# Optimization experiments

Hardware: AMD Instinct MI355X
Metric: run time of the kernel (lower is better)

Reference implementation:

```python
import jax, jax.numpy as jnp
import numpy as np

B, LQ, LK, D, H = 4, 2048, 2048, 768, 12
DH = D // H  # 64
EPS = 1e-5


def setup_inputs() -> dict:
    key = jax.random.key(0)
    ks = jax.random.split(key, 12)
    s = 0.02
    return {
        "queries": jax.random.normal(ks[0], (B, LQ, D), jnp.float32),
        "keys": jax.random.normal(ks[1], (B, LK, D), jnp.float32),
        "values": jax.random.normal(ks[2], (B, LK, D), jnp.float32),
        "mask": jax.random.randint(ks[3], (B, LK), 0, 2, jnp.int32),
        "Wq": jax.random.normal(ks[4], (D, D), jnp.float32) * s,
        "Wk": jax.random.normal(ks[5], (D, D), jnp.float32) * s,
        "Wv": jax.random.normal(ks[6], (D, D), jnp.float32) * s,
        "Wo": jax.random.normal(ks[7], (D, D), jnp.float32) * s,
        "W1": jax.random.normal(ks[8], (D, D), jnp.float32) * s,
        "b1": jnp.zeros((D,), jnp.float32),
        "W2": jax.random.normal(ks[9], (D, D), jnp.float32) * s,
        "b2": jnp.zeros((D,), jnp.float32),
        "ln_g": jnp.ones((D,), jnp.float32),
        "ln_b": jnp.zeros((D,), jnp.float32),
    }


def _split_heads(x):
    # [B, L, D] -> [B, H, L, DH]
    b, l, _ = x.shape
    return x.reshape(b, l, H, DH).transpose(0, 2, 1, 3)


def reference(queries, keys, values, mask, Wq, Wk, Wv, Wo, W1, b1, W2, b2, ln_g, ln_b):
    q = _split_heads(queries @ Wq)  # [B,H,LQ,DH]
    k = _split_heads(keys @ Wk)     # [B,H,LK,DH]
    v = _split_heads(values @ Wv)   # [B,H,LK,DH]

    scores = jnp.einsum("bhqd,bhkd->bhqk", q, k) / jnp.sqrt(jnp.float32(DH))

    # valid length per batch row = count of nonzero mask entries; positions >= valid_len are masked
    valid_lens = jnp.sum(mask != 0, axis=1)  # [B]
    key_ok = jnp.arange(LK, dtype=jnp.int32)[None, :] < valid_lens[:, None]  # [B,LK]
    scores = jnp.where(key_ok[:, None, None, :], scores, jnp.float32(-1e6))

    attn = jax.nn.softmax(scores, axis=-1)  # dropout is identity in eval
    out = jnp.einsum("bhqk,bhkd->bhqd", attn, v)  # [B,H,LQ,DH]
    out = out.transpose(0, 2, 1, 3).reshape(out.shape[0], out.shape[2], D)

    att_out = out @ Wo  # [B,LQ,D]
    ffn = jax.nn.relu(att_out @ W1 + b1) @ W2 + b2

    # residual + layernorm (torch code intends ln(dropout(ffn) + att_out))
    y = ffn + att_out
    mu = jnp.mean(y, axis=-1, keepdims=True)
    var = jnp.mean(jnp.square(y - mu), axis=-1, keepdims=True)
    return (y - mu) / jnp.sqrt(var + EPS) * ln_g + ln_b
```

## Files before the change

### kernel.cpp

```cpp
#include <hip/hip_runtime.h>
#include <stdint.h>

typedef __attribute__((ext_vector_type(4))) float floatx4;
typedef __attribute__((ext_vector_type(8))) __bf16 bf16x8;
typedef __attribute__((ext_vector_type(4))) __bf16 bf16x4;

#define DEV __device__ __forceinline__

constexpr int HB = 12;
constexpr int LSEQ = 2048;
constexpr int DMODEL = 768;
constexpr int MROWS = 8192;
constexpr float QSCALE = 0.125f * 1.44269504088896f;

DEV short f2bf(float f) {
  union { float f; uint32_t u; } x; x.f = f;
  uint32_t r = x.u + 0x7FFFu + ((x.u >> 16) & 1u);
  return (short)(r >> 16);
}

DEV float bf2f(short s) {
  union { uint32_t u; float f; } x; x.u = ((uint32_t)(uint16_t)s) << 16;
  return x.f;
}

typedef __attribute__((address_space(1))) void as1_void;
typedef __attribute__((address_space(3))) void as3_void;

DEV void gload_lds16(const void* g, void* l) {
  __builtin_amdgcn_global_load_lds((as1_void*)(uintptr_t)g, (as3_void*)l, 16, 0, 0);
}

__global__ __launch_bounds__(256)
void transpose_k(const float* w0, const float* w1, const float* w2,
                 const float* w3, const float* w4, const float* w5,
                 short* o0, short* o1, short* o2, short* o3, short* o4, short* o5)
{
  const float* W; short* O;
  switch (blockIdx.z) {
    case 0: W = w0; O = o0; break;
    case 1: W = w1; O = o1; break;
    case 2: W = w2; O = o2; break;
    case 3: W = w3; O = o3; break;
    case 4: W = w4; O = o4; break;
    default: W = w5; O = o5; break;
  }
  __shared__ float t[32][33];
  const int tx = threadIdx.x & 31, ty = threadIdx.x >> 5;
  const int n0 = blockIdx.x * 32, k0 = blockIdx.y * 32;
#pragma unroll
  for (int i = 0; i < 4; ++i)
    t[ty + i * 8][tx] = W[(size_t)(k0 + ty + i * 8) * DMODEL + n0 + tx];
  __syncthreads();
#pragma unroll
  for (int i = 0; i < 4; ++i)
    O[(size_t)(n0 + ty + i * 8) * DMODEL + k0 + tx] = f2bf(t[tx][ty + i * 8]);
}

__global__ __launch_bounds__(256)
void cvt_k(const float* __restrict__ s0, const float* __restrict__ s1, const float* __restrict__ s2,
           short* __restrict__ d0, short* __restrict__ d1, short* __restrict__ d2)
{
  const float* s; short* d;
  switch (blockIdx.y) { case 0: s = s0; d = d0; break; case 1: s = s1; d = d1; break; default: s = s2; d = d2; break; }
  const size_t i = ((size_t)blockIdx.x * 256 + threadIdx.x) * 4;
  const float4 v = *(const float4*)(s + i);
  short4 r; r.x = f2bf(v.x); r.y = f2bf(v.y); r.z = f2bf(v.z); r.w = f2bf(v.w);
  *(short4*)(d + i) = r;
}

__global__ __launch_bounds__(256)
void vlens_k(const int* __restrict__ mask, int* __restrict__ vl)
{
  const int b = blockIdx.x;
  int s = 0;
  for (int i = threadIdx.x; i < LSEQ; i += 256) s += (mask[b * LSEQ + i] != 0) ? 1 : 0;
#pragma unroll
  for (int o = 32; o >= 1; o >>= 1) s += __shfl_xor(s, o);
  __shared__ int red[4];
  const int lane = threadIdx.x & 63, wave = threadIdx.x >> 6;
  if (lane == 0) red[wave] = s;
  __syncthreads();
  if (threadIdx.x == 0) vl[b] = red[0] + red[1] + red[2] + red[3];
}

enum { EPI_QKV = 0, EPI_PLAIN = 2, EPI_BIAS_RELU = 3, EPI_Y = 4 };

template <int EPI>
__global__ __launch_bounds__(256)
void gemm_k(const short* __restrict__ A0, const short* __restrict__ A1, const short* __restrict__ A2,
            const short* __restrict__ B0, const short* __restrict__ B1, const short* __restrict__ B2,
            const float* __restrict__ bias, const short* __restrict__ resid,
            void* __restrict__ o0, void* __restrict__ o1, void* __restrict__ o2)
{
  __shared__ __align__(16) short As[2][2][64 * 32];
  __shared__ __align__(16) short Bs[2][2][128 * 32];
  const short* A = A0;
  const short* Bt = B0;
  if constexpr (EPI == EPI_QKV) {
    if (blockIdx.z == 1) { A = A1; Bt = B1; }
    else if (blockIdx.z == 2) { A = A2; Bt = B2; }
  }
  const int tid = threadIdx.x;
  const int lane = tid & 63, wave = tid >> 6;
  const int wm = wave >> 1, wn = wave & 1;
  const int m0 = blockIdx.x * 64, n0 = blockIdx.y * 128;
  const int col = lane & 15, quad = lane >> 4;
  const int sr = lane >> 2;
  const int sk = (lane & 3) * 8;

  const short* Arow = A + (size_t)(m0 + wave * 16 + sr) * DMODEL + sk;
  const short* Brow0 = Bt + (size_t)(n0 + (wave * 2 + 0) * 16 + sr) * DMODEL + sk;
  const short* Brow1 = Bt + (size_t)(n0 + (wave * 2 + 1) * 16 + sr) * DMODEL + sk;

  auto stage = [&](int kt, int buf) {
    const int k0 = kt * 64;
#pragma unroll
    for (int h = 0; h < 2; ++h) {
      gload_lds16(Arow + k0 + h * 32, &As[buf][h][wave * 512]);
      gload_lds16(Brow0 + k0 + h * 32, &Bs[buf][h][(wave * 2 + 0) * 512]);
      gload_lds16(Brow1 + k0 + h * 32, &Bs[buf][h][(wave * 2 + 1) * 512]);
    }
  };

  floatx4 acc[2][4] = {};

  stage(0, 0);
  for (int kt = 0; kt < 12; ++kt) {
    const int cur = kt & 1;
    asm volatile("s_barrier" ::: "memory");
    if (kt + 1 < 12) {
      stage(kt + 1, cur ^ 1);
      asm volatile("s_waitcnt vmcnt(6)" ::: "memory");
    } else {
      asm volatile("s_waitcnt vmcnt(0)" ::: "memory");
    }
    asm volatile("s_barrier" ::: "memory");
#pragma unroll
    for (int h = 0; h < 2; ++h) {
      bf16x8 af[2], bfr[4];
#pragma unroll
      for (int t = 0; t < 2; ++t)
        af[t] = *(const bf16x8*)&As[cur][h][(wm * 32 + t * 16 + col) * 32 + quad * 8];
#pragma unroll
      for (int t = 0; t < 4; ++t)
        bfr[t] = *(const bf16x8*)&Bs[cur][h][(wn * 64 + t * 16 + col) * 32 + quad * 8];
#pragma unroll
      for (int mt = 0; mt < 2; ++mt)
#pragma unroll
        for (int nt = 0; nt < 4; ++nt)
          acc[mt][nt] = __builtin_amdgcn_mfma_f32_16x16x32_bf16(af[mt], bfr[nt], acc[mt][nt], 0, 0, 0);
    }
  }

#pragma unroll
  for (int mt = 0; mt < 2; ++mt) {
#pragma unroll
    for (int nt = 0; nt < 4; ++nt) {
#pragma unroll
      for (int r = 0; r < 4; ++r) {
        const int m = m0 + wm * 32 + mt * 16 + quad * 4 + r;
        const int n = n0 + wn * 64 + nt * 16 + col;
        float v = acc[mt][nt][r];
        if constexpr (EPI == EPI_QKV) {
          const int b = m >> 11, l = m & 2047, h = n >> 6, dh = n & 63;
          const int z = blockIdx.z;
          if (z == 0) {
            ((short*)o0)[((size_t)(b * HB + h) * LSEQ + l) * 64 + dh] = f2bf(v * QSCALE);
          } else if (z == 1) {
            ((short*)o1)[((size_t)(b * HB + h) * LSEQ + l) * 64 + dh] = f2bf(v);
          } else {
            ((short*)o2)[((size_t)(b * HB + h) * 64 + dh) * LSEQ + l] = f2bf(v);
          }
        } else if constexpr (EPI == EPI_PLAIN) {
          ((short*)o0)[(size_t)m * DMODEL + n] = f2bf(v);
        } else if constexpr (EPI == EPI_BIAS_RELU) {
          v += bias[n]; v = v > 0.f ? v : 0.f;
          ((short*)o0)[(size_t)m * DMODEL + n] = f2bf(v);
        } else {
          v += bias[n] + bf2f(resid[(size_t)m * DMODEL + n]);
          ((float*)o0)[(size_t)m * DMODEL + n] = v;
        }
      }
    }
  }
}

constexpr int PSP = 68;
__global__ __launch_bounds__(256)
void attn_k(const short* __restrict__ qw, const short* __restrict__ kw, const short* __restrict__ vtw,
            const int* __restrict__ vlens, short* __restrict__ outp)
{
  __shared__ __align__(16) short Qs[2][128][32];
  __shared__ __align__(16) short Ks[2][64][32];
  __shared__ __align__(16) short Vts[2][64][32];
  __shared__ __align__(16) short Ps[4][32 * PSP];

  const int tid = threadIdx.x;
  const int lane = tid & 63, wave = tid >> 6;
  const int col = lane & 15, quad = lane >> 4;
  const int bh = blockIdx.x, b = bh / HB, h = bh % HB;
  const int q0 = blockIdx.y * 128;
  const int vl = vlens[b];
  const int sr = lane >> 2, sk = (lane & 3) * 8;

  const short* qbase = qw  + (size_t)bh * LSEQ * 64;
  const short* kbase = kw  + (size_t)bh * LSEQ * 64;
  const short* vbase = vtw + (size_t)bh * 64 * LSEQ;

#pragma unroll
  for (int i = 0; i < 4; ++i) {
    const int c = wave * 4 + i;
    const int hs = c >> 3, r0 = (c & 7) * 16;
    gload_lds16(qbase + (size_t)(q0 + r0 + sr) * 64 + hs * 32 + sk, &Qs[hs][r0][0]);
  }

  floatx4 oacc[2][4] = {};
  float li[2][4] = {};

  const int ktend = (vl > 0) ? ((vl + 63) >> 6) : (LSEQ / 64);

  for (int kt = 0; kt < ktend; ++kt) {
    __syncthreads();
#pragma unroll
    for (int i = 0; i < 2; ++i) {
      const int c = wave * 2 + i;
      const int hs = c >> 2, r0 = (c & 3) * 16;
      gload_lds16(kbase + (size_t)(kt * 64 + r0 + sr) * 64 + hs * 32 + sk, &Ks[hs][r0][0]);
      gload_lds16(vbase + (size_t)(r0 + sr) * LSEQ + kt * 64 + hs * 32 + sk, &Vts[hs][r0][0]);
    }
    __syncthreads();

    floatx4 sacc[2][4] = {};
#pragma unroll
    for (int ks = 0; ks < 2; ++ks) {
      bf16x8 aq[2], bk[4];
#pragma unroll
      for (int mt = 0; mt < 2; ++mt)
        aq[mt] = *(const bf16x8*)&Qs[ks][wave * 32 + mt * 16 + col][quad * 8];
#pragma unroll
      for (int nt = 0; nt < 4; ++nt)
        bk[nt] = *(const bf16x8*)&Ks[ks][nt * 16 + col][quad * 8];
#pragma unroll
      for (int mt = 0; mt < 2; ++mt)
#pragma unroll
        for (int nt = 0; nt < 4; ++nt)
          sacc[mt][nt] = __builtin_amdgcn_mfma_f32_16x16x32_bf16(aq[mt], bk[nt], sacc[mt][nt], 0, 0, 0);
    }

    if (kt * 64 + 64 > vl) {
#pragma unroll
      for (int nt = 0; nt < 4; ++nt) {
        const bool ok = (kt * 64 + nt * 16 + col) < vl;
#pragma unroll
        for (int mt = 0; mt < 2; ++mt)
#pragma unroll
          for (int r = 0; r < 4; ++r)
            sacc[mt][nt][r] = ok ? sacc[mt][nt][r] : -1.0e6f;
      }
    }

#pragma unroll
    for (int mt = 0; mt < 2; ++mt)
#pragma unroll
      for (int nt = 0; nt < 4; ++nt)
#pragma unroll
        for (int r = 0; r < 4; ++r) {
          const float p = __builtin_amdgcn_exp2f(sacc[mt][nt][r]);
          li[mt][r] += p;
          union { float f; uint32_t u; } pu; pu.f = p;
          Ps[wave][(mt * 16 + quad * 4 + r) * PSP + nt * 16 + col] =
              (short)((pu.u + 0x8000u) >> 16);
        }

    asm volatile("s_waitcnt lgkmcnt(0)" ::: "memory");

#pragma unroll
    for (int ks = 0; ks < 2; ++ks) {
      bf16x8 ap[2], bv[4];
#pragma unroll
      for (int mt = 0; mt < 2; ++mt) {
        union { bf16x8 v8; bf16x4 v4[2]; } u;
        const short* base = &Ps[wave][(mt * 16 + col) * PSP + ks * 32 + quad * 8];
        u.v4[0] = *(const bf16x4*)base;
        u.v4[1] = *(const bf16x4*)(base + 4);
        ap[mt] = u.v8;
      }
#pragma unroll
      for (int nt = 0; nt < 4; ++nt)
        bv[nt] = *(const bf16x8*)&Vts[ks][nt * 16 + col][quad * 8];
#pragma unroll
      for (int mt = 0; mt < 2; ++mt)
#pragma unroll
        for (int nt = 0; nt < 4; ++nt)
          oacc[mt][nt] = __builtin_amdgcn_mfma_f32_16x16x32_bf16(ap[mt], bv[nt], oacc[mt][nt], 0, 0, 0);
    }
  }

  float rli[2][4];
#pragma unroll
  for (int mt = 0; mt < 2; ++mt)
#pragma unroll
    for (int r = 0; r < 4; ++r) {
      float t = li[mt][r];
      t += __shfl_xor(t, 1); t += __shfl_xor(t, 2);
      t += __shfl_xor(t, 4); t += __shfl_xor(t, 8);
      rli[mt][r] = 1.0f / fmaxf(t, 1e-30f);
    }

#pragma unroll
  for (int mt = 0; mt < 2; ++mt)
#pragma unroll
    for (int nt = 0; nt < 4; ++nt)
#pragma unroll
      for (int r = 0; r < 4; ++r) {
        const int qrow = q0 + wave * 32 + mt * 16 + quad * 4 + r;
        const int dh = nt * 16 + col;
        const float v = oacc[mt][nt][r] * rli[mt][r];
        outp[((size_t)b * LSEQ + qrow) * DMODEL + h * 64 + dh] = f2bf(v);
      }
}

__global__ __launch_bounds__(256)
void ln_k(const float* __restrict__ y, const float* __restrict__ g, const float* __restrict__ be,
          float* __restrict__ o)
{
  const int row = blockIdx.x;
  const int tid = threadIdx.x;
  const float* yr = y + (size_t)row * DMODEL;
  float v[3];
  float s = 0.f, sq = 0.f;
#pragma unroll
  for (int i = 0; i < 3; ++i) { v[i] = yr[tid + i * 256]; s += v[i]; sq += v[i] * v[i]; }
#pragma unroll
  for (int off = 32; off >= 1; off >>= 1) { s += __shfl_xor(s, off); sq += __shfl_xor(sq, off); }
  __shared__ float red[8];
  const int lane = tid & 63, wave = tid >> 6;
  if (lane == 0) { red[wave] = s; red[4 + wave] = sq; }
  __syncthreads();
  s = red[0] + red[1] + red[2] + red[3];
  sq = red[4] + red[5] + red[6] + red[7];
  const float mu = s * (1.f / 768.f);
  const float var = sq * (1.f / 768.f) - mu * mu;
  const float rstd = rsqrtf(var + 1e-5f);
  float* orow = o + (size_t)row * DMODEL;
#pragma unroll
  for (int i = 0; i < 3; ++i) {
    const int c = tid + i * 256;
    orow[c] = (v[i] - mu) * rstd * g[c] + be[c];
  }
}

extern "C" void kernel_launch(void* const* d_in, const int* in_sizes, int n_in,
                              void* d_out, int out_size, void* d_ws, size_t ws_size,
                              hipStream_t stream)
{
  const float* queries = (const float*)d_in[0];
  const float* keys    = (const float*)d_in[1];
  const float* values  = (const float*)d_in[2];
  const int*   mask    = (const int*)d_in[3];
  const float* Wq = (const float*)d_in[4];
  const float* Wk = (const float*)d_in[5];
  const float* Wv = (const float*)d_in[6];
  const float* Wo = (const float*)d_in[7];
  const float* W1 = (const float*)d_in[8];
  const float* b1 = (const float*)d_in[9];
  const float* W2 = (const float*)d_in[10];
  const float* b2 = (const float*)d_in[11];
  const float* ln_g = (const float*)d_in[12];
  const float* ln_b = (const float*)d_in[13];

  char* ws = (char*)d_ws;
  size_t off = 0;
  auto alloc = [&](size_t bytes) -> void* {
    void* p = ws + off;
    off = (off + bytes + 255) & ~(size_t)255;
    return p;
  };
  int* vlens = (int*)alloc(256);
  short* wt[6];
  for (int i = 0; i < 6; ++i) wt[i] = (short*)alloc((size_t)DMODEL * DMODEL * 2);
  constexpr size_t SB = (size_t)MROWS * DMODEL * 2;
  short* xq  = (short*)alloc(SB);
  short* xk  = (short*)alloc(SB);
  short* xv  = (short*)alloc(SB);
  short* qw  = (short*)alloc(SB);
  short* kw  = (short*)alloc(SB);
  short* vtw = (short*)alloc(SB);
  short* attn_cat = xq;
  short* atto_bf  = xk;
  short* h1       = xv;
  float* yb       = (float*)qw;

  dim3 blk(256);
  transpose_k<<<dim3(24, 24, 6), blk, 0, stream>>>(Wq, Wk, Wv, Wo, W1, W2,
                                                   wt[0], wt[1], wt[2], wt[3], wt[4], wt[5]);
  cvt_k<<<dim3(6144, 3), blk, 0, stream>>>(queries, keys, values, xq, xk, xv);
  vlens_k<<<dim3(4), blk, 0, stream>>>(mask, vlens);
  gemm_k<EPI_QKV><<<dim3(128, 6, 3), blk, 0, stream>>>(
      xq, xk, xv, wt[0], wt[1], wt[2], nullptr, nullptr, qw, kw, vtw);
  attn_k<<<dim3(48, 16), blk, 0, stream>>>(qw, kw, vtw, vlens, attn_cat);
  gemm_k<EPI_PLAIN><<<dim3(128, 6, 1), blk, 0, stream>>>(
      attn_cat, nullptr, nullptr, wt[3], nullptr, nullptr, nullptr, nullptr,
      atto_bf, nullptr, nullptr);
  gemm_k<EPI_BIAS_RELU><<<dim3(128, 6, 1), blk, 0, stream>>>(
      atto_bf, nullptr, nullptr, wt[4], nullptr, nullptr, b1, nullptr,
      h1, nullptr, nullptr);
  gemm_k<EPI_Y><<<dim3(128, 6, 1), blk, 0, stream>>>(
      h1, nullptr, nullptr, wt[5], nullptr, nullptr, b2, atto_bf,
      yb, nullptr, nullptr);
  ln_k<<<dim3(MROWS), blk, 0, stream>>>(yb, ln_g, ln_b, (float*)d_out);
}
```

Baseline: 332.6 us.

## Keep P in registers via transposed S MFMA and double-buffer K/V tiles

The attention kernel now computes S transposed (K as the A operand, Q as B), so each lane holds four consecutive keys for one query. Those values are packed to bf16 and fed straight into 16x16x16 MFMAs against V^T, which removes the P round-trip through shared memory. K/V tiles are double-buffered with a prefetch of the next tile and raw barriers plus vmcnt waits, so global loads overlap with compute. Output is stored as 4-wide vectors. The risks are the smaller-K MFMA (more instructions), higher register pressure, and the correctness of the hand-placed waitcnt and barrier sequence.

```diff
diff --git a/kernel.cpp b/kernel.cpp
--- a/kernel.cpp
+++ b/kernel.cpp
@@ -3,7 +3,7 @@
 
 typedef __attribute__((ext_vector_type(4))) float floatx4;
 typedef __attribute__((ext_vector_type(8))) __bf16 bf16x8;
-typedef __attribute__((ext_vector_type(4))) __bf16 bf16x4;
+typedef __attribute__((ext_vector_type(4))) short short4v;
 
 #define DEV __device__ __forceinline__
 
@@ -186,15 +186,13 @@
   }
 }
 
-constexpr int PSP = 68;
 __global__ __launch_bounds__(256)
 void attn_k(const short* __restrict__ qw, const short* __restrict__ kw, const short* __restrict__ vtw,
             const int* __restrict__ vlens, short* __restrict__ outp)
 {
   __shared__ __align__(16) short Qs[2][128][32];
-  __shared__ __align__(16) short Ks[2][64][32];
-  __shared__ __align__(16) short Vts[2][64][32];
-  __shared__ __align__(16) short Ps[4][32 * PSP];
+  __shared__ __align__(16) short Ks[2][2][64][32];
+  __shared__ __align__(16) short Vts[2][2][64][32];
 
   const int tid = threadIdx.x;
   const int lane = tid & 63, wave = tid >> 6;
@@ -215,110 +213,118 @@
     gload_lds16(qbase + (size_t)(q0 + r0 + sr) * 64 + hs * 32 + sk, &Qs[hs][r0][0]);
   }
 
-  floatx4 oacc[2][4] = {};
-  float li[2][4] = {};
-
-  const int ktend = (vl > 0) ? ((vl + 63) >> 6) : (LSEQ / 64);
-
-  for (int kt = 0; kt < ktend; ++kt) {
-    __syncthreads();
+  auto stage = [&](int kt, int buf) {
 #pragma unroll
     for (int i = 0; i < 2; ++i) {
       const int c = wave * 2 + i;
       const int hs = c >> 2, r0 = (c & 3) * 16;
-      gload_lds16(kbase + (size_t)(kt * 64 + r0 + sr) * 64 + hs * 32 + sk, &Ks[hs][r0][0]);
-      gload_lds16(vbase + (size_t)(r0 + sr) * LSEQ + kt * 64 + hs * 32 + sk, &Vts[hs][r0][0]);
-    }
-    __syncthreads();
-
-    floatx4 sacc[2][4] = {};
+      gload_lds16(kbase + (size_t)(kt * 64 + r0 + sr) * 64 + hs * 32 + sk, &Ks[buf][hs][r0][0]);
+      gload_lds16(vbase + (size_t)(r0 + sr) * LSEQ + kt * 64 + hs * 32 + sk, &Vts[buf][hs][r0][0]);
+    }
+  };
+
+  floatx4 oacc[4][2] = {};
+  float li[2] = {};
+
+  const int ktend = (vl > 0) ? ((vl + 63) >> 6) : (LSEQ / 64);
+
+  stage(0, 0);
+  for (int kt = 0; kt < ktend; ++kt) {
+    const int cur = kt & 1;
+    asm volatile("s_barrier" ::: "memory");
+    if (kt + 1 < ktend) {
+      stage(kt + 1, cur ^ 1);
+      asm volatile("s_waitcnt vmcnt(4)" ::: "memory");
+    } else {
+      asm volatile("s_waitcnt vmcnt(0)" ::: "memory");
+    }
+    asm volatile("s_barrier" ::: "memory");
+
+    floatx4 sacc[4][2] = {};
 #pragma unroll
     for (int ks = 0; ks < 2; ++ks) {
-      bf16x8 aq[2], bk[4];
-#pragma unroll
-      for (int mt = 0; mt < 2; ++mt)
-        aq[mt] = *(const bf16x8*)&Qs[ks][wave * 32 + mt * 16 + col][quad * 8];
-#pragma unroll
-      for (int nt = 0; nt < 4; ++nt)
-        bk[nt] = *(const bf16x8*)&Ks[ks][nt * 16 + col][quad * 8];
-#pragma unroll
-      for (int mt = 0; mt < 2; ++mt)
-#pragma unroll
-        for (int nt = 0; nt < 4; ++nt)
-          sacc[mt][nt] = __builtin_amdgcn_mfma_f32_16x16x32_bf16(aq[mt], bk[nt], sacc[mt][nt], 0, 0, 0);
+      bf16x8 kf[4], qf[2];
+#pragma unroll
+      for (int kc = 0; kc < 4; ++kc)
+        kf[kc] = *(const bf16x8*)&Ks[cur][ks][kc * 16 + col][quad * 8];
+#pragma unroll
+      for (int qc = 0; qc < 2; ++qc)
+        qf[qc] = *(const bf16x8*)&Qs[ks][wave * 32 + qc * 16 + col][quad * 8];
+#pragma unroll
+      for (int kc = 0; kc < 4; ++kc)
+#pragma unroll
+        for (int qc = 0; qc < 2; ++qc)
+          sacc[kc][qc] = __builtin_amdgcn_mfma_f32_16x16x32_bf16(kf[kc], qf[qc], sacc[kc][qc], 0, 0, 0);
     }
 
     if (kt * 64 + 64 > vl) {
 #pragma unroll
-      for (int nt = 0; nt < 4; ++nt) {
-        const bool ok = (kt * 64 + nt * 16 + col) < vl;
-#pragma unroll
-        for (int mt = 0; mt < 2; ++mt)
-#pragma unroll
-          for (int r = 0; r < 4; ++r)
-            sacc[mt][nt][r] = ok ? sacc[mt][nt][r] : -1.0e6f;
+      for (int kc = 0; kc < 4; ++kc) {
+        const int pbase = kt * 64 + kc * 16 + quad * 4;
+#pragma unroll
+        for (int r = 0; r < 4; ++r) {
+          const bool ok = (pbase + r) < vl;
+#pragma unroll
+          for (int qc = 0; qc < 2; ++qc)
+            sacc[kc][qc][r] = ok ? sacc[kc][qc][r] : -1.0e6f;
+        }
       }
     }
 
-#pragma unroll
-    for (int mt = 0; mt < 2; ++mt)
-#pragma unroll
-      for (int nt = 0; nt < 4; ++nt)
-#pragma unroll
-        for (int r = 0; r < 4; ++r) {
-          const float p = __builtin_amdgcn_exp2f(sacc[mt][nt][r]);
-          li[mt][r] += p;
-          union { float f; uint32_t u; } pu; pu.f = p;
-          Ps[wave][(mt * 16 + quad * 4 + r) * PSP + nt * 16 + col] =
-              (short)((pu.u + 0x8000u) >> 16);
-        }
-
-    asm volatile("s_waitcnt lgkmcnt(0)" ::: "memory");
-
-#pragma unroll
-    for (int ks = 0; ks < 2; ++ks) {
-      bf16x8 ap[2], bv[4];
-#pragma unroll
-      for (int mt = 0; mt < 2; ++mt) {
-        union { bf16x8 v8; bf16x4 v4[2]; } u;
-        const short* base = &Ps[wave][(mt * 16 + col) * PSP + ks * 32 + quad * 8];
-        u.v4[0] = *(const bf16x4*)base;
-        u.v4[1] = *(const bf16x4*)(base + 4);
-        ap[mt] = u.v8;
+    short4v pf[4][2];
+#pragma unroll
+    for (int kc = 0; kc < 4; ++kc)
+#pragma unroll
+      for (int qc = 0; qc < 2; ++qc) {
+        union { float f; uint32_t u; } p0, p1, p2, p3;
+        p0.f = __builtin_amdgcn_exp2f(sacc[kc][qc][0]);
+        p1.f = __builtin_amdgcn_exp2f(sacc[kc][qc][1]);
+        p2.f = __builtin_amdgcn_exp2f(sacc[kc][qc][2]);
+        p3.f = __builtin_amdgcn_exp2f(sacc[kc][qc][3]);
+        li[qc] += (p0.f + p1.f) + (p2.f + p3.f);
+        union { int2 i2; short4v s4; } pk;
+        pk.i2.x = (int)__builtin_amdgcn_perm(p1.u, p0.u, 0x07060302u);
+        pk.i2.y = (int)__builtin_amdgcn_perm(p3.u, p2.u, 0x07060302u);
+        pf[kc][qc] = pk.s4;
       }
-#pragma unroll
-      for (int nt = 0; nt < 4; ++nt)
-        bv[nt] = *(const bf16x8*)&Vts[ks][nt * 16 + col][quad * 8];
-#pragma unroll
-      for (int mt = 0; mt < 2; ++mt)
-#pragma unroll
-        for (int nt = 0; nt < 4; ++nt)
-          oacc[mt][nt] = __builtin_amdgcn_mfma_f32_16x16x32_bf16(ap[mt], bv[nt], oacc[mt][nt], 0, 0, 0);
-    }
-  }
-
-  float rli[2][4];
-#pragma unroll
-  for (int mt = 0; mt < 2; ++mt)
-#pragma unroll
-    for (int r = 0; r < 4; ++r) {
-      float t = li[mt][r];
-      t += __shfl_xor(t, 1); t += __shfl_xor(t, 2);
-      t += __shfl_xor(t, 4); t += __shfl_xor(t, 8);
-      rli[mt][r] = 1.0f / fmaxf(t, 1e-30f);
-    }
-
-#pragma unroll
-  for (int mt = 0; mt < 2; ++mt)
-#pragma unroll
-    for (int nt = 0; nt < 4; ++nt)
-#pragma unroll
-      for (int r = 0; r < 4; ++r) {
-        const int qrow = q0 + wave * 32 + mt * 16 + quad * 4 + r;
-        const int dh = nt * 16 + col;
-        const float v = oacc[mt][nt][r] * rli[mt][r];
-        outp[((size_t)b * LSEQ + qrow) * DMODEL + h * 64 + dh] = f2bf(v);
-      }
+
+#pragma unroll
+    for (int nt = 0; nt < 4; ++nt) {
+      short4v vf[4];
+#pragma unroll
+      for (int kc = 0; kc < 4; ++kc)
+        vf[kc] = *(const short4v*)&Vts[cur][kc >> 1][nt * 16 + col][(kc & 1) * 16 + quad * 4];
+#pragma unroll
+      for (int qc = 0; qc < 2; ++qc)
+#pragma unroll
+        for (int kc = 0; kc < 4; ++kc)
+          oacc[nt][qc] = __builtin_amdgcn_mfma_f32_16x16x16bf16_1k(vf[kc], pf[kc][qc], oacc[nt][qc], 0, 0, 0);
+    }
+  }
+
+  float rli[2];
+#pragma unroll
+  for (int qc = 0; qc < 2; ++qc) {
+    float t = li[qc];
+    t += __shfl_xor(t, 16);
+    t += __shfl_xor(t, 32);
+    rli[qc] = 1.0f / fmaxf(t, 1e-30f);
+  }
+
+#pragma unroll
+  for (int qc = 0; qc < 2; ++qc) {
+    const int q = q0 + wave * 32 + qc * 16 + col;
+    short* orow = outp + ((size_t)b * LSEQ + q) * DMODEL + h * 64 + quad * 4;
+#pragma unroll
+    for (int nt = 0; nt < 4; ++nt) {
+      short4 s;
+      s.x = f2bf(oacc[nt][qc][0] * rli[qc]);
+      s.y = f2bf(oacc[nt][qc][1] * rli[qc]);
+      s.z = f2bf(oacc[nt][qc][2] * rli[qc]);
+      s.w = f2bf(oacc[nt][qc][3] * rli[qc]);
+      *(short4*)(orow + nt * 16) = s;
+    }
+  }
 }
 
 __global__ __launch_bounds__(256)
```

After: 332.2 us. About the same (-0.1%).
